# Kernel tuning notes

Hardware: AMD Instinct MI355X
Metric: run time of the kernel (lower is better)

Reference implementation:

```python
import jax, jax.numpy as jnp
import numpy as np

IN_FEATURES = 4096
OUT_FEATURES = 14336
TOKENS = 32


def setup_inputs() -> dict:
    key = jax.random.key(0)
    k1, k2, k3 = jax.random.split(key, 3)
    x = jax.random.normal(k1, (TOKENS, IN_FEATURES), dtype=jnp.float32)
    # int8-valued quantized weight stored as int32 (symmetric Q8, range [-127, 127])
    weight = jax.random.randint(k2, (OUT_FEATURES, IN_FEATURES), -127, 128, dtype=jnp.int32)
    # per-in-feature (per-column of [out,in] matrix) positive scales
    scales = jax.random.uniform(k3, (IN_FEATURES,), dtype=jnp.float32, minval=0.001, maxval=0.02)
    return {"x": x, "weight": weight, "scales": scales}


def reference(x, weight, scales):
    # Original torch: dequant[o,i] = weight[o,i] * scales[i]; out = x @ dequant.T
    # Equivalent fused form: out[t,o] = sum_i (x[t,i]*scales[i]) * weight[o,i]
    x_scaled = x * scales[None, :]            # [T, in]
    w = weight.astype(jnp.float32)            # [out, in]
    out = jnp.einsum('ti,oi->to', x_scaled, w)  # [T, out]
    return out
```

## Files before the change

### kernel.cpp

```cpp
#include <hip/hip_runtime.h>
#include <stdint.h>
#include <stddef.h>

#define IN_F   4096
#define OUT_F  14336
#define TOK    32

#define OTILE  64
#define ISPLIT 4
#define IBLK   (IN_F / ISPLIT)
#define ICHUNK 64
#define NCHUNK (IBLK / ICHUNK)

typedef const __attribute__((address_space(1))) void* gas_ptr;
typedef __attribute__((address_space(3))) void* las_ptr;

__global__ __launch_bounds__(256) void prep_kernel(
    const float* __restrict__ x, const float* __restrict__ scales,
    float* __restrict__ xsT, float* __restrict__ out)
{
    const int f = blockIdx.x * 256 + threadIdx.x;
    const int i = f >> 5;
    const int t = f & 31;
    xsT[f] = x[(size_t)t * IN_F + i] * scales[i];
    if (f < (OUT_F * TOK / 4)) {
        ((float4*)out)[f] = make_float4(0.f, 0.f, 0.f, 0.f);
    }
}

__global__ __launch_bounds__(256, 4) void qgemm_kernel(
    const int* __restrict__ wgt, const float* __restrict__ xsT,
    float* __restrict__ out)
{
    __shared__ int lds[2][OTILE * ICHUNK];
    const int lane = threadIdx.x & 63;
    const int wv   = __builtin_amdgcn_readfirstlane(threadIdx.x >> 6);
    const int o0   = blockIdx.x * OTILE;
    const int ib0  = blockIdx.y * IBLK;
    const int lx   = lane & 15;

    float acc[8];
#pragma unroll
    for (int t = 0; t < 8; ++t) acc[t] = 0.f;

    auto stage = [&](int buf, int c) {
#pragma unroll
        for (int k = 0; k < 4; ++k) {
            const int m = wv * 4 + k;
            const int r = m * 4 + (lane >> 4);
            const int j = lx ^ (r & 15);
            const int* g = wgt + (size_t)(o0 + r) * IN_F
                               + (ib0 + c * ICHUNK) + (j << 2);
            int* l = &lds[buf][m * 256];
            __builtin_amdgcn_global_load_lds((gas_ptr)g, (las_ptr)l, 16, 0, 0);
        }
    };

    stage(0, 0);
    __syncthreads();

    int cur = 0;
    for (int c = 0; c < NCHUNK; ++c) {
        if (c + 1 < NCHUNK) stage(cur ^ 1, c + 1);

        const int* row = &lds[cur][lane * ICHUNK];
        const float* xs_base = xsT + (size_t)(ib0 + c * ICHUNK) * TOK + wv * 8;
#pragma unroll
        for (int q = 0; q < 16; ++q) {
            const int4 wq = *(const int4*)(row + ((q ^ lx) << 2));
            const float f0 = (float)wq.x;
            const float f1 = (float)wq.y;
            const float f2 = (float)wq.z;
            const float f3 = (float)wq.w;
            const float* xsp = xs_base + q * 4 * TOK;
#pragma unroll
            for (int t = 0; t < 8; ++t) {
                float a = acc[t];
                a = fmaf(f0, xsp[t],           a);
                a = fmaf(f1, xsp[TOK + t],     a);
                a = fmaf(f2, xsp[2 * TOK + t], a);
                a = fmaf(f3, xsp[3 * TOK + t], a);
                acc[t] = a;
            }
        }
        __syncthreads();
        cur ^= 1;
    }

#pragma unroll
    for (int t = 0; t < 8; ++t) {
        atomicAdd(&out[(size_t)(wv * 8 + t) * OUT_F + o0 + lane], acc[t]);
    }
}

extern "C" void kernel_launch(void* const* d_in, const int* in_sizes, int n_in,
                              void* d_out, int out_size, void* d_ws, size_t ws_size,
                              hipStream_t stream)
{
    const float* x      = (const float*)d_in[0];
    const int*   wgt    = (const int*)d_in[1];
    const float* scales = (const float*)d_in[2];
    float* out = (float*)d_out;
    float* xsT = (float*)d_ws;

    prep_kernel<<<dim3((TOK * IN_F) / 256), 256, 0, stream>>>(x, scales, xsT, out);

    dim3 grid(OUT_F / OTILE, ISPLIT);
    qgemm_kernel<<<grid, 256, 0, stream>>>(wgt, xsT, out);
}
```

Before: 365.4 us.

## Use bf16 MFMA for int-weight GEMM with prepacked activation fragments

Replaces the scalar FP32 FMA inner loop with bf16 16x16x32 MFMA instructions. Weights are converted int→float→bf16 by truncation, which is exact for int8 values. The prep kernel now scales activations, rounds them to bf16 and packs them into MFMA A-fragment layout, and each block holds these fragments in registers. The input split is raised from 4 to 16, giving more blocks and more atomics. Activation precision drops from fp32 to bf16, which may affect tolerance.

```diff
diff --git a/kernel.cpp b/kernel.cpp
--- a/kernel.cpp
+++ b/kernel.cpp
@@ -7,90 +7,128 @@
 #define TOK    32
 
 #define OTILE  64
-#define ISPLIT 4
+#define ISPLIT 16
 #define IBLK   (IN_F / ISPLIT)
 #define ICHUNK 64
 #define NCHUNK (IBLK / ICHUNK)
+#define KBPB   (IBLK / 32)
 
 typedef const __attribute__((address_space(1))) void* gas_ptr;
 typedef __attribute__((address_space(3))) void* las_ptr;
+typedef __attribute__((ext_vector_type(8))) short bf16x8;
+typedef __attribute__((ext_vector_type(4))) float f32x4;
 
 __global__ __launch_bounds__(256) void prep_kernel(
     const float* __restrict__ x, const float* __restrict__ scales,
-    float* __restrict__ xsT, float* __restrict__ out)
+    int4* __restrict__ xfrag, float* __restrict__ out)
 {
     const int f = blockIdx.x * 256 + threadIdx.x;
-    const int i = f >> 5;
-    const int t = f & 31;
-    xsT[f] = x[(size_t)t * IN_F + i] * scales[i];
+    if (f < (TOK * IN_F / 8)) {
+        const int t  = f >> 9;
+        const int i8 = f & 511;
+        const int kb = i8 >> 2;
+        const int kg = i8 & 3;
+        const float4* xp = (const float4*)(x + (size_t)t * IN_F + i8 * 8);
+        const float4* sp = (const float4*)(scales + i8 * 8);
+        float4 x0 = xp[0], x1 = xp[1];
+        float4 s0 = sp[0], s1 = sp[1];
+        float v[8] = { x0.x*s0.x, x0.y*s0.y, x0.z*s0.z, x0.w*s0.w,
+                       x1.x*s1.x, x1.y*s1.y, x1.z*s1.z, x1.w*s1.w };
+        uint32_t h[8];
+#pragma unroll
+        for (int j = 0; j < 8; ++j) {
+            uint32_t b = __float_as_uint(v[j]);
+            b += 0x7fffu + ((b >> 16) & 1u);
+            h[j] = b >> 16;
+        }
+        int4 d;
+        d.x = (int)(h[0] | (h[1] << 16));
+        d.y = (int)(h[2] | (h[3] << 16));
+        d.z = (int)(h[4] | (h[5] << 16));
+        d.w = (int)(h[6] | (h[7] << 16));
+        xfrag[((kb * 2 + (t >> 4)) * 64) + kg * 16 + (t & 15)] = d;
+    }
     if (f < (OUT_F * TOK / 4)) {
         ((float4*)out)[f] = make_float4(0.f, 0.f, 0.f, 0.f);
     }
 }
 
 __global__ __launch_bounds__(256, 4) void qgemm_kernel(
-    const int* __restrict__ wgt, const float* __restrict__ xsT,
+    const int* __restrict__ wgt, const int4* __restrict__ xfrag,
     float* __restrict__ out)
 {
-    __shared__ int lds[2][OTILE * ICHUNK];
+    __shared__ int wtile[2][OTILE * ICHUNK];
     const int lane = threadIdx.x & 63;
-    const int wv   = __builtin_amdgcn_readfirstlane(threadIdx.x >> 6);
+    const int wv   = threadIdx.x >> 6;
+    const int wvu  = __builtin_amdgcn_readfirstlane(wv);
     const int o0   = blockIdx.x * OTILE;
     const int ib0  = blockIdx.y * IBLK;
     const int lx   = lane & 15;
+    const int quad = lane >> 4;
 
-    float acc[8];
+    int4 a[KBPB][2];
 #pragma unroll
-    for (int t = 0; t < 8; ++t) acc[t] = 0.f;
+    for (int kb = 0; kb < KBPB; ++kb)
+#pragma unroll
+        for (int mt = 0; mt < 2; ++mt)
+            a[kb][mt] = xfrag[((blockIdx.y * KBPB + kb) * 2 + mt) * 64 + lane];
 
     auto stage = [&](int buf, int c) {
 #pragma unroll
         for (int k = 0; k < 4; ++k) {
-            const int m = wv * 4 + k;
+            const int m = wvu * 4 + k;
             const int r = m * 4 + (lane >> 4);
             const int j = lx ^ (r & 15);
             const int* g = wgt + (size_t)(o0 + r) * IN_F
                                + (ib0 + c * ICHUNK) + (j << 2);
-            int* l = &lds[buf][m * 256];
+            int* l = &wtile[buf][m * 256];
             __builtin_amdgcn_global_load_lds((gas_ptr)g, (las_ptr)l, 16, 0, 0);
         }
     };
+
+    f32x4 acc[2] = { {0.f,0.f,0.f,0.f}, {0.f,0.f,0.f,0.f} };
 
     stage(0, 0);
     __syncthreads();
 
     int cur = 0;
+#pragma unroll
     for (int c = 0; c < NCHUNK; ++c) {
         if (c + 1 < NCHUNK) stage(cur ^ 1, c + 1);
 
-        const int* row = &lds[cur][lane * ICHUNK];
-        const float* xs_base = xsT + (size_t)(ib0 + c * ICHUNK) * TOK + wv * 8;
+        const int* rowp = &wtile[cur][(wvu * 16 + lx) * ICHUNK];
 #pragma unroll
-        for (int q = 0; q < 16; ++q) {
-            const int4 wq = *(const int4*)(row + ((q ^ lx) << 2));
-            const float f0 = (float)wq.x;
-            const float f1 = (float)wq.y;
-            const float f2 = (float)wq.z;
-            const float f3 = (float)wq.w;
-            const float* xsp = xs_base + q * 4 * TOK;
-#pragma unroll
-            for (int t = 0; t < 8; ++t) {
-                float a = acc[t];
-                a = fmaf(f0, xsp[t],           a);
-                a = fmaf(f1, xsp[TOK + t],     a);
-                a = fmaf(f2, xsp[2 * TOK + t], a);
-                a = fmaf(f3, xsp[3 * TOK + t], a);
-                acc[t] = a;
-            }
+        for (int kb2 = 0; kb2 < 2; ++kb2) {
+            const int g0 = kb2 * 8 + quad * 2;
+            const int4 w0 = *(const int4*)(rowp + ((g0 ^ lx) << 2));
+            const int4 w1 = *(const int4*)(rowp + (((g0 + 1) ^ lx) << 2));
+            bf16x8 b;
+            b[0] = (short)(__float_as_uint((float)w0.x) >> 16);
+            b[1] = (short)(__float_as_uint((float)w0.y) >> 16);
+            b[2] = (short)(__float_as_uint((float)w0.z) >> 16);
+            b[3] = (short)(__float_as_uint((float)w0.w) >> 16);
+            b[4] = (short)(__float_as_uint((float)w1.x) >> 16);
+            b[5] = (short)(__float_as_uint((float)w1.y) >> 16);
+            b[6] = (short)(__float_as_uint((float)w1.z) >> 16);
+            b[7] = (short)(__float_as_uint((float)w1.w) >> 16);
+            const int kbl = c * 2 + kb2;
+            bf16x8 a0, a1;
+            __builtin_memcpy(&a0, &a[kbl][0], 16);
+            __builtin_memcpy(&a1, &a[kbl][1], 16);
+            acc[0] = __builtin_amdgcn_mfma_f32_16x16x32_bf16(a0, b, acc[0], 0, 0, 0);
+            acc[1] = __builtin_amdgcn_mfma_f32_16x16x32_bf16(a1, b, acc[1], 0, 0, 0);
         }
         __syncthreads();
         cur ^= 1;
     }
 
 #pragma unroll
-    for (int t = 0; t < 8; ++t) {
-        atomicAdd(&out[(size_t)(wv * 8 + t) * OUT_F + o0 + lane], acc[t]);
-    }
+    for (int mt = 0; mt < 2; ++mt)
+#pragma unroll
+        for (int reg = 0; reg < 4; ++reg) {
+            const int t = mt * 16 + quad * 4 + reg;
+            atomicAdd(&out[(size_t)t * OUT_F + o0 + wvu * 16 + lx], acc[mt][reg]);
+        }
 }
 
 extern "C" void kernel_launch(void* const* d_in, const int* in_sizes, int n_in,
@@ -101,10 +139,10 @@
     const int*   wgt    = (const int*)d_in[1];
     const float* scales = (const float*)d_in[2];
     float* out = (float*)d_out;
-    float* xsT = (float*)d_ws;
+    int4*  xfrag = (int4*)d_ws;
 
-    prep_kernel<<<dim3((TOK * IN_F) / 256), 256, 0, stream>>>(x, scales, xsT, out);
+    prep_kernel<<<dim3((TOK * IN_F) / 256), 256, 0, stream>>>(x, scales, xfrag, out);
 
     dim3 grid(OUT_F / OTILE, ISPLIT);
-    qgemm_kernel<<<grid, 256, 0, stream>>>(wgt, xsT, out);
+    qgemm_kernel<<<grid, 256, 0, stream>>>(wgt, xfrag, out);
 }
```

After: 328.5 us. 1.11x faster.
